# Optimization experiments

Measured on AMD Instinct MI355X. Metric: run time of the kernel, lower is better.

The kernel has to match this reference:

```python
import jax, jax.numpy as jnp
import numpy as np

N_NODES = 10000
N_EDGES = 100000
IN_FEATS = 64
OUT_FEATS = 64
N_EDGE_TYPES = 10


def setup_inputs() -> dict:
    key = jax.random.key(0)
    k_feat, k_src, k_dst, k_ord, k_emb = jax.random.split(key, 5)
    feat = jax.random.normal(k_feat, (N_NODES, IN_FEATS), dtype=jnp.float32)
    src = jax.random.randint(k_src, (N_EDGES,), 0, N_NODES, dtype=jnp.int32)
    dst = jax.random.randint(k_dst, (N_EDGES,), 0, N_NODES, dtype=jnp.int32)
    order = jax.random.randint(k_ord, (N_EDGES,), 0, N_EDGE_TYPES, dtype=jnp.int32)
    # xavier-uniform-like init for the relation-weight embedding table
    emb_weight = jax.random.normal(k_emb, (N_EDGE_TYPES, IN_FEATS * OUT_FEATS), dtype=jnp.float32) * 0.02
    bias = jnp.zeros((OUT_FEATS,), dtype=jnp.float32)
    return {"feat": feat, "src": src, "dst": dst, "order": order,
            "emb_weight": emb_weight, "bias": bias}


def reference(feat, src, dst, order, emb_weight, bias):
    n_nodes, in_feats = feat.shape
    out_feats = emb_weight.shape[1] // in_feats
    n_edges = src.shape[0]
    ones_e = jnp.ones((n_edges,), dtype=feat.dtype)

    # norm='both': scale source features by out_degree^{-1/2}
    out_deg = jnp.clip(jax.ops.segment_sum(ones_e, src, num_segments=n_nodes), 1.0)
    feat_n = feat * (out_deg ** -0.5)[:, None]

    # per-edge relation weight gather: [E, out, in]
    w = emb_weight[order].reshape(n_edges, out_feats, in_feats)
    h_src = feat_n[src]                              # [E, in]
    msg = jnp.einsum('eoi,ei->eo', w, h_src)         # [E, out]

    # scatter-sum aggregate to destination nodes
    rst = jax.ops.segment_sum(msg, dst, num_segments=n_nodes)  # [N, out]

    # post-norm by in_degree^{-1/2}
    in_deg = jnp.clip(jax.ops.segment_sum(ones_e, dst, num_segments=n_nodes), 1.0)
    rst = rst * (in_deg ** -0.5)[:, None]
    return rst + bias
```

## Files before the change

### kernel.cpp

```cpp
#include <hip/hip_runtime.h>
#include <stdint.h>


typedef __attribute__((ext_vector_type(8))) short short8;
typedef __attribute__((ext_vector_type(4))) float f32x4;

constexpr int N_NODES = 10000;
constexpr int N_EDGES = 100000;
constexpr int F = 64;
constexpr int R = 10;
constexpr int BLOCK = 256;
constexpr int MAX_GROUPS = (N_EDGES + 16 * R) / 16 + 1;

union U8 { uint32_t u[4]; short8 s; };

__device__ inline uint32_t pk_hi(float x, float y) {
    uint32_t bx = __float_as_uint(x), by = __float_as_uint(y);
    return (bx >> 16) | (by & 0xFFFF0000u);
}
__device__ inline uint32_t pk_lo(float x, float y) {
    uint32_t bx = __float_as_uint(x), by = __float_as_uint(y);
    float lx = x - __uint_as_float(bx & 0xFFFF0000u);
    float ly = y - __uint_as_float(by & 0xFFFF0000u);
    return (__float_as_uint(lx) >> 16) | (__float_as_uint(ly) & 0xFFFF0000u);
}

__global__ void k_count(const int* __restrict__ src, const int* __restrict__ dst,
                        const int* __restrict__ order,
                        int* deg_out, int* deg_in, int* rel_cnt, int* rank,
                        int* done, int* start_p) {
    __shared__ int hist[R], base[R];
    int tid = threadIdx.x;
    int e = blockIdx.x * BLOCK + tid;
    if (tid < R) hist[tid] = 0;
    __syncthreads();
    int r = -1, lr = 0;
    if (e < N_EDGES) {
        atomicAdd(&deg_out[src[e]], 1);
        atomicAdd(&deg_in[dst[e]], 1);
        r = order[e];
        lr = atomicAdd(&hist[r], 1);
    }
    __syncthreads();
    if (tid < R) base[tid] = hist[tid] ? atomicAdd(&rel_cnt[tid], hist[tid]) : 0;
    __syncthreads();
    if (e < N_EDGES) rank[e] = base[r] + lr;

    if (tid == 0) {
        __threadfence();
        if (atomicAdd(done, 1) == (int)gridDim.x - 1) {
            int off = 0;
            for (int rr = 0; rr < R; ++rr) {
                start_p[rr] = off;
                int c = atomicAdd(&rel_cnt[rr], 0);
                off += (c + 15) & ~15;
            }
            start_p[R] = off;
        }
    }
}

__global__ void k_prep(const int* __restrict__ src, const int* __restrict__ dst,
                       const int* __restrict__ order, const int* __restrict__ rank,
                       const int* __restrict__ start_p, const int* __restrict__ rel_cnt,
                       const int* __restrict__ deg_out,
                       const float* __restrict__ feat, const float* __restrict__ emb,
                       int2* __restrict__ sd, float* __restrict__ featn,
                       uint4* __restrict__ wfrag, float* __restrict__ out) {
    int t = blockIdx.x * BLOCK + threadIdx.x;
    if (t < N_NODES * F) {
        featn[t] = feat[t] * rsqrtf((float)max(deg_out[t >> 6], 1));
        out[t] = 0.0f;
    }
    if (t < N_EDGES)
        sd[start_p[order[t]] + rank[t]] = make_int2(src[t], dst[t]);
    if (t < R * 16) {
        int r = t >> 4, i = t & 15;
        int slot = start_p[r] + rel_cnt[r] + i;
        if (slot < start_p[r + 1]) sd[slot] = make_int2(0, -1);
    }
    if (t < R * 16 * 64) {
        int lane = t & 63, frag = t >> 6;
        int p = frag & 1, s = (frag >> 1) & 1, tt = (frag >> 2) & 3, r = frag >> 4;
        int o = 16 * tt + (lane & 15), q = lane >> 4;
        const float* w = emb + (size_t)r * F * F + (size_t)o * F + 32 * s + 8 * q;
        float4 f0 = *(const float4*)w;
        float4 f1 = *(const float4*)(w + 4);
        uint4 v;
        if (p == 0) v = make_uint4(pk_hi(f0.x, f0.y), pk_hi(f0.z, f0.w),
                                   pk_hi(f1.x, f1.y), pk_hi(f1.z, f1.w));
        else        v = make_uint4(pk_lo(f0.x, f0.y), pk_lo(f0.z, f0.w),
                                   pk_lo(f1.x, f1.y), pk_lo(f1.z, f1.w));
        wfrag[(size_t)frag * 64 + lane] = v;
    }
}

__global__ __launch_bounds__(BLOCK, 4) void k_edge(
    const float* __restrict__ featn, const short8* __restrict__ wfrag,
    const int* __restrict__ start_p, const int2* __restrict__ sd,
    float* __restrict__ out) {
    int lane = threadIdx.x & 63;
    int wib = threadIdx.x >> 6;
    int g = blockIdx.x * (BLOCK / 64) + wib;
    int e0 = g * 16;
    int pend = start_p[R];
    if (e0 >= pend) return;
    int r = 0;
    while (start_p[r + 1] <= e0) ++r;

    int2 m = sd[e0 + (lane & 15)];
    int q = lane >> 4;

    const float* arow = featn + (size_t)m.x * F + 8 * q;
    float4 f0 = *(const float4*)arow;
    float4 f1 = *(const float4*)(arow + 4);
    float4 f2 = *(const float4*)(arow + 32);
    float4 f3 = *(const float4*)(arow + 36);
    U8 ah0, al0, ah1, al1;
    ah0.u[0] = pk_hi(f0.x, f0.y); ah0.u[1] = pk_hi(f0.z, f0.w);
    ah0.u[2] = pk_hi(f1.x, f1.y); ah0.u[3] = pk_hi(f1.z, f1.w);
    al0.u[0] = pk_lo(f0.x, f0.y); al0.u[1] = pk_lo(f0.z, f0.w);
    al0.u[2] = pk_lo(f1.x, f1.y); al0.u[3] = pk_lo(f1.z, f1.w);
    ah1.u[0] = pk_hi(f2.x, f2.y); ah1.u[1] = pk_hi(f2.z, f2.w);
    ah1.u[2] = pk_hi(f3.x, f3.y); ah1.u[3] = pk_hi(f3.z, f3.w);
    al1.u[0] = pk_lo(f2.x, f2.y); al1.u[1] = pk_lo(f2.z, f2.w);
    al1.u[2] = pk_lo(f3.x, f3.y); al1.u[3] = pk_lo(f3.z, f3.w);

    const short8* wf = wfrag + (size_t)r * 16 * 64;
    f32x4 acc[4];
#pragma unroll
    for (int t = 0; t < 4; ++t) acc[t] = (f32x4){0.f, 0.f, 0.f, 0.f};

#pragma unroll
    for (int t = 0; t < 4; ++t) {
        short8 bh0 = wf[(t * 4 + 0) * 64 + lane];
        short8 bl0 = wf[(t * 4 + 1) * 64 + lane];
        short8 bh1 = wf[(t * 4 + 2) * 64 + lane];
        short8 bl1 = wf[(t * 4 + 3) * 64 + lane];
        f32x4 a = acc[t];
        a = __builtin_amdgcn_mfma_f32_16x16x32_bf16(al0.s, bh0, a, 0, 0, 0);
        a = __builtin_amdgcn_mfma_f32_16x16x32_bf16(ah0.s, bl0, a, 0, 0, 0);
        a = __builtin_amdgcn_mfma_f32_16x16x32_bf16(ah0.s, bh0, a, 0, 0, 0);
        a = __builtin_amdgcn_mfma_f32_16x16x32_bf16(al1.s, bh1, a, 0, 0, 0);
        a = __builtin_amdgcn_mfma_f32_16x16x32_bf16(ah1.s, bl1, a, 0, 0, 0);
        a = __builtin_amdgcn_mfma_f32_16x16x32_bf16(ah1.s, bh1, a, 0, 0, 0);
        acc[t] = a;
    }

#pragma unroll
    for (int gg = 0; gg < 4; ++gg) {
        int row = q * 4 + gg;
        int drow = __shfl(m.y, row);
        if (drow >= 0) {
#pragma unroll
            for (int t = 0; t < 4; ++t)
                unsafeAtomicAdd(&out[(size_t)drow * F + 16 * t + (lane & 15)], acc[t][gg]);
        }
    }
}

__global__ void k_final(const int* __restrict__ deg_in, const float* __restrict__ bias,
                        float* __restrict__ out) {
    int t = blockIdx.x * BLOCK + threadIdx.x;
    if (t < N_NODES * F / 4) {
        int n = t >> 4, o4 = t & 15;
        float s = rsqrtf((float)max(deg_in[n], 1));
        float4 v = ((float4*)out)[t];
        float4 b = ((const float4*)bias)[o4];
        v.x = v.x * s + b.x; v.y = v.y * s + b.y;
        v.z = v.z * s + b.z; v.w = v.w * s + b.w;
        ((float4*)out)[t] = v;
    }
}

extern "C" void kernel_launch(void* const* d_in, const int* in_sizes, int n_in,
                              void* d_out, int out_size, void* d_ws, size_t ws_size,
                              hipStream_t stream) {
    const float* feat  = (const float*)d_in[0];
    const int*   src   = (const int*)d_in[1];
    const int*   dst   = (const int*)d_in[2];
    const int*   order = (const int*)d_in[3];
    const float* emb   = (const float*)d_in[4];
    const float* bias  = (const float*)d_in[5];
    float* out = (float*)d_out;

    int*   base_i   = (int*)d_ws;
    int*   deg_out  = base_i;
    int*   deg_in   = deg_out + N_NODES;
    int*   rel_cnt  = deg_in + N_NODES;
    int*   done     = rel_cnt + 16;
    int*   start_p  = done + 16;
    int*   rank     = start_p + 32;
    int2*  sd       = (int2*)(rank + N_EDGES);
    float* featn    = (float*)(sd + (N_EDGES + 16 * R));
    uint4* wfrag    = (uint4*)(featn + N_NODES * F);

    size_t zbytes = (size_t)(2 * N_NODES + 64) * sizeof(int);
    hipMemsetAsync(d_ws, 0, zbytes, stream);

    int eb = (N_EDGES + BLOCK - 1) / BLOCK;
    k_count<<<eb, BLOCK, 0, stream>>>(src, dst, order, deg_out, deg_in,
                                      rel_cnt, rank, done, start_p);
    int pb = (N_NODES * F + BLOCK - 1) / BLOCK;
    k_prep<<<pb, BLOCK, 0, stream>>>(src, dst, order, rank, start_p, rel_cnt,
                                     deg_out, feat, emb, sd, featn, wfrag, out);
    int gwaves = MAX_GROUPS;
    int gblocks = (gwaves + (BLOCK / 64) - 1) / (BLOCK / 64);
    k_edge<<<gblocks, BLOCK, 0, stream>>>(featn, (const short8*)wfrag, start_p, sd, out);
    k_final<<<(N_NODES * F / 4 + BLOCK - 1) / BLOCK, BLOCK, 0, stream>>>(deg_in, bias, out);
}
```

Baseline: 119.9 us.

## Fuse source normalization into edge kernel and process 32 edges per wave

Removes the featn intermediate by applying the out-degree rsqrt scaling inside the edge kernel when building A fragments, and moves output zeroing into the count kernel, which shrinks k_prep to one block per 256 edges. Each wave now handles two 16-edge tiles, reusing the weight fragment loads and interleaving independent MFMA chains. This cuts a full-feature write and read pass at the cost of more registers (launch bounds lowered to 3) and more padding per relation.

```diff
diff --git a/kernel.cpp b/kernel.cpp
--- a/kernel.cpp
+++ b/kernel.cpp
@@ -10,7 +10,8 @@
 constexpr int F = 64;
 constexpr int R = 10;
 constexpr int BLOCK = 256;
-constexpr int MAX_GROUPS = (N_EDGES + 16 * R) / 16 + 1;
+constexpr int EPG = 32;
+constexpr int MAX_GROUPS = (N_EDGES + EPG * R) / EPG + 1;
 
 union U8 { uint32_t u[4]; short8 s; };
 
@@ -28,10 +29,12 @@
 __global__ void k_count(const int* __restrict__ src, const int* __restrict__ dst,
                         const int* __restrict__ order,
                         int* deg_out, int* deg_in, int* rel_cnt, int* rank,
-                        int* done, int* start_p) {
+                        int* done, int* start_p, float4* __restrict__ outv) {
     __shared__ int hist[R], base[R];
     int tid = threadIdx.x;
     int e = blockIdx.x * BLOCK + tid;
+    for (int i = e; i < N_NODES * F / 4; i += gridDim.x * BLOCK)
+        outv[i] = make_float4(0.f, 0.f, 0.f, 0.f);
     if (tid < R) hist[tid] = 0;
     __syncthreads();
     int r = -1, lr = 0;
@@ -53,7 +56,7 @@
             for (int rr = 0; rr < R; ++rr) {
                 start_p[rr] = off;
                 int c = atomicAdd(&rel_cnt[rr], 0);
-                off += (c + 15) & ~15;
+                off += (c + EPG - 1) & ~(EPG - 1);
             }
             start_p[R] = off;
         }
@@ -63,19 +66,13 @@
 __global__ void k_prep(const int* __restrict__ src, const int* __restrict__ dst,
                        const int* __restrict__ order, const int* __restrict__ rank,
                        const int* __restrict__ start_p, const int* __restrict__ rel_cnt,
-                       const int* __restrict__ deg_out,
-                       const float* __restrict__ feat, const float* __restrict__ emb,
-                       int2* __restrict__ sd, float* __restrict__ featn,
-                       uint4* __restrict__ wfrag, float* __restrict__ out) {
+                       const float* __restrict__ emb,
+                       int2* __restrict__ sd, uint4* __restrict__ wfrag) {
     int t = blockIdx.x * BLOCK + threadIdx.x;
-    if (t < N_NODES * F) {
-        featn[t] = feat[t] * rsqrtf((float)max(deg_out[t >> 6], 1));
-        out[t] = 0.0f;
-    }
     if (t < N_EDGES)
         sd[start_p[order[t]] + rank[t]] = make_int2(src[t], dst[t]);
-    if (t < R * 16) {
-        int r = t >> 4, i = t & 15;
+    if (t < R * EPG) {
+        int r = t / EPG, i = t % EPG;
         int slot = start_p[r] + rel_cnt[r] + i;
         if (slot < start_p[r + 1]) sd[slot] = make_int2(0, -1);
     }
@@ -95,41 +92,57 @@
     }
 }
 
-__global__ __launch_bounds__(BLOCK, 4) void k_edge(
-    const float* __restrict__ featn, const short8* __restrict__ wfrag,
-    const int* __restrict__ start_p, const int2* __restrict__ sd,
-    float* __restrict__ out) {
+__device__ inline void mk_afrag(const float* __restrict__ feat,
+                                const int* __restrict__ deg_out,
+                                int srow, int q,
+                                U8& h0, U8& l0, U8& h1, U8& l1) {
+    float nr = rsqrtf((float)max(deg_out[srow], 1));
+    const float* row = feat + (size_t)srow * F + 8 * q;
+    float4 f0 = *(const float4*)row;
+    float4 f1 = *(const float4*)(row + 4);
+    float4 f2 = *(const float4*)(row + 32);
+    float4 f3 = *(const float4*)(row + 36);
+    f0.x *= nr; f0.y *= nr; f0.z *= nr; f0.w *= nr;
+    f1.x *= nr; f1.y *= nr; f1.z *= nr; f1.w *= nr;
+    f2.x *= nr; f2.y *= nr; f2.z *= nr; f2.w *= nr;
+    f3.x *= nr; f3.y *= nr; f3.z *= nr; f3.w *= nr;
+    h0.u[0] = pk_hi(f0.x, f0.y); h0.u[1] = pk_hi(f0.z, f0.w);
+    h0.u[2] = pk_hi(f1.x, f1.y); h0.u[3] = pk_hi(f1.z, f1.w);
+    l0.u[0] = pk_lo(f0.x, f0.y); l0.u[1] = pk_lo(f0.z, f0.w);
+    l0.u[2] = pk_lo(f1.x, f1.y); l0.u[3] = pk_lo(f1.z, f1.w);
+    h1.u[0] = pk_hi(f2.x, f2.y); h1.u[1] = pk_hi(f2.z, f2.w);
+    h1.u[2] = pk_hi(f3.x, f3.y); h1.u[3] = pk_hi(f3.z, f3.w);
+    l1.u[0] = pk_lo(f2.x, f2.y); l1.u[1] = pk_lo(f2.z, f2.w);
+    l1.u[2] = pk_lo(f3.x, f3.y); l1.u[3] = pk_lo(f3.z, f3.w);
+}
+
+__global__ __launch_bounds__(BLOCK, 3) void k_edge(
+    const float* __restrict__ feat, const int* __restrict__ deg_out,
+    const short8* __restrict__ wfrag, const int* __restrict__ start_p,
+    const int2* __restrict__ sd, float* __restrict__ out) {
     int lane = threadIdx.x & 63;
     int wib = threadIdx.x >> 6;
     int g = blockIdx.x * (BLOCK / 64) + wib;
-    int e0 = g * 16;
-    int pend = start_p[R];
-    if (e0 >= pend) return;
+    int e0 = g * EPG;
+    if (e0 >= start_p[R]) return;
     int r = 0;
     while (start_p[r + 1] <= e0) ++r;
 
-    int2 m = sd[e0 + (lane & 15)];
     int q = lane >> 4;
-
-    const float* arow = featn + (size_t)m.x * F + 8 * q;
-    float4 f0 = *(const float4*)arow;
-    float4 f1 = *(const float4*)(arow + 4);
-    float4 f2 = *(const float4*)(arow + 32);
-    float4 f3 = *(const float4*)(arow + 36);
-    U8 ah0, al0, ah1, al1;
-    ah0.u[0] = pk_hi(f0.x, f0.y); ah0.u[1] = pk_hi(f0.z, f0.w);
-    ah0.u[2] = pk_hi(f1.x, f1.y); ah0.u[3] = pk_hi(f1.z, f1.w);
-    al0.u[0] = pk_lo(f0.x, f0.y); al0.u[1] = pk_lo(f0.z, f0.w);
-    al0.u[2] = pk_lo(f1.x, f1.y); al0.u[3] = pk_lo(f1.z, f1.w);
-    ah1.u[0] = pk_hi(f2.x, f2.y); ah1.u[1] = pk_hi(f2.z, f2.w);
-    ah1.u[2] = pk_hi(f3.x, f3.y); ah1.u[3] = pk_hi(f3.z, f3.w);
-    al1.u[0] = pk_lo(f2.x, f2.y); al1.u[1] = pk_lo(f2.z, f2.w);
-    al1.u[2] = pk_lo(f3.x, f3.y); al1.u[3] = pk_lo(f3.z, f3.w);
+    int2 mA = sd[e0 + (lane & 15)];
+    int2 mB = sd[e0 + 16 + (lane & 15)];
+
+    U8 Ah0, Al0, Ah1, Al1, Bh0, Bl0, Bh1, Bl1;
+    mk_afrag(feat, deg_out, mA.x, q, Ah0, Al0, Ah1, Al1);
+    mk_afrag(feat, deg_out, mB.x, q, Bh0, Bl0, Bh1, Bl1);
 
     const short8* wf = wfrag + (size_t)r * 16 * 64;
-    f32x4 acc[4];
-#pragma unroll
-    for (int t = 0; t < 4; ++t) acc[t] = (f32x4){0.f, 0.f, 0.f, 0.f};
+    f32x4 acc0[4], acc1[4];
+#pragma unroll
+    for (int t = 0; t < 4; ++t) {
+        acc0[t] = (f32x4){0.f, 0.f, 0.f, 0.f};
+        acc1[t] = (f32x4){0.f, 0.f, 0.f, 0.f};
+    }
 
 #pragma unroll
     for (int t = 0; t < 4; ++t) {
@@ -137,24 +150,37 @@
         short8 bl0 = wf[(t * 4 + 1) * 64 + lane];
         short8 bh1 = wf[(t * 4 + 2) * 64 + lane];
         short8 bl1 = wf[(t * 4 + 3) * 64 + lane];
-        f32x4 a = acc[t];
-        a = __builtin_amdgcn_mfma_f32_16x16x32_bf16(al0.s, bh0, a, 0, 0, 0);
-        a = __builtin_amdgcn_mfma_f32_16x16x32_bf16(ah0.s, bl0, a, 0, 0, 0);
-        a = __builtin_amdgcn_mfma_f32_16x16x32_bf16(ah0.s, bh0, a, 0, 0, 0);
-        a = __builtin_amdgcn_mfma_f32_16x16x32_bf16(al1.s, bh1, a, 0, 0, 0);
-        a = __builtin_amdgcn_mfma_f32_16x16x32_bf16(ah1.s, bl1, a, 0, 0, 0);
-        a = __builtin_amdgcn_mfma_f32_16x16x32_bf16(ah1.s, bh1, a, 0, 0, 0);
-        acc[t] = a;
-    }
-
+        f32x4 x = acc0[t], y = acc1[t];
+        x = __builtin_amdgcn_mfma_f32_16x16x32_bf16(Al0.s, bh0, x, 0, 0, 0);
+        y = __builtin_amdgcn_mfma_f32_16x16x32_bf16(Bl0.s, bh0, y, 0, 0, 0);
+        x = __builtin_amdgcn_mfma_f32_16x16x32_bf16(Ah0.s, bl0, x, 0, 0, 0);
+        y = __builtin_amdgcn_mfma_f32_16x16x32_bf16(Bh0.s, bl0, y, 0, 0, 0);
+        x = __builtin_amdgcn_mfma_f32_16x16x32_bf16(Ah0.s, bh0, x, 0, 0, 0);
+        y = __builtin_amdgcn_mfma_f32_16x16x32_bf16(Bh0.s, bh0, y, 0, 0, 0);
+        x = __builtin_amdgcn_mfma_f32_16x16x32_bf16(Al1.s, bh1, x, 0, 0, 0);
+        y = __builtin_amdgcn_mfma_f32_16x16x32_bf16(Bl1.s, bh1, y, 0, 0, 0);
+        x = __builtin_amdgcn_mfma_f32_16x16x32_bf16(Ah1.s, bl1, x, 0, 0, 0);
+        y = __builtin_amdgcn_mfma_f32_16x16x32_bf16(Bh1.s, bl1, y, 0, 0, 0);
+        x = __builtin_amdgcn_mfma_f32_16x16x32_bf16(Ah1.s, bh1, x, 0, 0, 0);
+        y = __builtin_amdgcn_mfma_f32_16x16x32_bf16(Bh1.s, bh1, y, 0, 0, 0);
+        acc0[t] = x; acc1[t] = y;
+    }
+
+    int col = lane & 15;
 #pragma unroll
     for (int gg = 0; gg < 4; ++gg) {
         int row = q * 4 + gg;
-        int drow = __shfl(m.y, row);
-        if (drow >= 0) {
+        int dA = __shfl(mA.y, row);
+        int dB = __shfl(mB.y, row);
+        if (dA >= 0) {
 #pragma unroll
             for (int t = 0; t < 4; ++t)
-                unsafeAtomicAdd(&out[(size_t)drow * F + 16 * t + (lane & 15)], acc[t][gg]);
+                unsafeAtomicAdd(&out[(size_t)dA * F + 16 * t + col], acc0[t][gg]);
+        }
+        if (dB >= 0) {
+#pragma unroll
+            for (int t = 0; t < 4; ++t)
+                unsafeAtomicAdd(&out[(size_t)dB * F + 16 * t + col], acc1[t][gg]);
         }
     }
 }
@@ -184,28 +210,25 @@
     const float* bias  = (const float*)d_in[5];
     float* out = (float*)d_out;
 
-    int*   base_i   = (int*)d_ws;
-    int*   deg_out  = base_i;
+    int*   deg_out  = (int*)d_ws;
     int*   deg_in   = deg_out + N_NODES;
     int*   rel_cnt  = deg_in + N_NODES;
     int*   done     = rel_cnt + 16;
     int*   start_p  = done + 16;
     int*   rank     = start_p + 32;
     int2*  sd       = (int2*)(rank + N_EDGES);
-    float* featn    = (float*)(sd + (N_EDGES + 16 * R));
-    uint4* wfrag    = (uint4*)(featn + N_NODES * F);
+    uint4* wfrag    = (uint4*)(sd + (N_EDGES + EPG * R));
 
     size_t zbytes = (size_t)(2 * N_NODES + 64) * sizeof(int);
     hipMemsetAsync(d_ws, 0, zbytes, stream);
 
     int eb = (N_EDGES + BLOCK - 1) / BLOCK;
     k_count<<<eb, BLOCK, 0, stream>>>(src, dst, order, deg_out, deg_in,
-                                      rel_cnt, rank, done, start_p);
-    int pb = (N_NODES * F + BLOCK - 1) / BLOCK;
-    k_prep<<<pb, BLOCK, 0, stream>>>(src, dst, order, rank, start_p, rel_cnt,
-                                     deg_out, feat, emb, sd, featn, wfrag, out);
-    int gwaves = MAX_GROUPS;
-    int gblocks = (gwaves + (BLOCK / 64) - 1) / (BLOCK / 64);
-    k_edge<<<gblocks, BLOCK, 0, stream>>>(featn, (const short8*)wfrag, start_p, sd, out);
+                                      rel_cnt, rank, done, start_p, (float4*)out);
+    k_prep<<<eb, BLOCK, 0, stream>>>(src, dst, order, rank, start_p, rel_cnt,
+                                     emb, sd, wfrag);
+    int gblocks = (MAX_GROUPS + (BLOCK / 64) - 1) / (BLOCK / 64);
+    k_edge<<<gblocks, BLOCK, 0, stream>>>(feat, deg_out, (const short8*)wfrag,
+                                          start_p, sd, out);
     k_final<<<(N_NODES * F / 4 + BLOCK - 1) / BLOCK, BLOCK, 0, stream>>>(deg_in, bias, out);
 }
```

Result: no change. 118.4 us (-1.3%).
